# Kernel tuning notes

Hardware: AMD Instinct MI355X
Metric: run time of the kernel (lower is better)

Reference implementation:

```python
import jax, jax.numpy as jnp
import numpy as np

S = 2        # downscale
REDUCE = 32  # QK channel dim


def _to_grid(x):
    # [B,C,H,W] -> [B,C,H/S,W/S,S*S], matching ConverToGrid (reshape+permute+reshape)
    B, C, H, W = x.shape
    h, w = H // S, W // S
    x = x.reshape(B, C, h, S, w, S)
    x = x.transpose(0, 1, 2, 4, 3, 5)
    return x.reshape(B, C, h, w, S * S)


def setup_inputs() -> dict:
    key = jax.random.key(0)
    k1, k2, k3 = jax.random.split(key, 3)
    fm = jax.random.normal(k1, (8, 128, 256, 256), dtype=jnp.float32)
    Wq = jax.random.normal(k2, (REDUCE, 128), dtype=jnp.float32) * 0.05
    Wk = jax.random.normal(k3, (REDUCE, 128), dtype=jnp.float32) * 0.05
    return {"fm": fm, "Wq": Wq, "Wk": Wk}


def reference(fm, Wq, Wk):
    B, C, H, W = fm.shape
    h, w = H // S, W // S
    # Q branch: AvgPool2d(S,S) -> 1x1 conv -> scale by 1/sqrt(reduce)
    pooled = fm.reshape(B, C, h, S, w, S).mean(axis=(3, 5))          # [B,C,h,w]
    Q = jnp.einsum('rc,bchw->brhw', Wq, pooled) / jnp.sqrt(
        jnp.asarray(REDUCE, fm.dtype))                               # [B,r,h,w]
    # K branch: 1x1 conv -> grid
    K = _to_grid(jnp.einsum('rc,bchw->brhw', Wk, fm))                # [B,r,h,w,S*S]
    # V branch: grid of raw features
    V = _to_grid(fm)                                                 # [B,C,h,w,S*S]
    # sum over channel dim of Q*K, softmax over window dim (dropout p=0 => identity)
    logits = jnp.einsum('brhw,brhws->bhws', Q, K)                    # [B,h,w,S*S]
    attn = jax.nn.softmax(logits, axis=-1)
    # weighted sum over window positions
    out = jnp.einsum('bchws,bhws->bchw', V, attn)                    # [B,C,h,w]
    return out
```

## Files before the change

kernel.cpp:

```cpp
#include <hip/hip_runtime.h>
#include <hip/hip_bf16.h>
#include <math.h>


typedef unsigned int uint32;

__device__ __forceinline__ uint32 pack2(float x, float y) {
  union { __hip_bfloat162 h; uint32 u; } cvt;
  cvt.h = __float22bfloat162_rn(make_float2(x, y));
  return cvt.u;
}
__device__ __forceinline__ float2 unpack2(uint32 u) {
  float2 r;
  r.x = __uint_as_float(u << 16);
  r.y = __uint_as_float(u & 0xffff0000u);
  return r;
}

__global__ __launch_bounds__(256) void wt_kernel(const float* __restrict__ Wq,
                                                 const float* __restrict__ Wk,
                                                 float* __restrict__ ws) {
  int t = blockIdx.x * 256 + threadIdx.x;
  if (t < 4096) {
    int c = t >> 5, r = t & 31;
    ws[c * 32 + r]        = Wq[r * 128 + c] * (0.25f / sqrtf(32.0f));
    ws[4096 + c * 32 + r] = Wk[r * 128 + c];
  }
}

__global__ __launch_bounds__(256)
void attn_main(const float* __restrict__ fm,
               const float* __restrict__ ws,
               float* __restrict__ out) {
  __shared__ uint2 stash[128][64];
  __shared__ float lbuf[4][64][4];
  __shared__ float abuf[64][4];

  const int tid = threadIdx.x;
  const int p   = tid & 63;
  const int w   = __builtin_amdgcn_readfirstlane(tid >> 6);

  const int blk = blockIdx.x;
  const int w0  = (blk & 1) * 64;
  const int h   = (blk >> 1) & 127;
  const int b   = blk >> 8;

  const float* g = fm + ((size_t)(b * 128)) * 65536 +
                   (size_t)(2 * h) * 256 + 2 * (w0 + p);
  const float* wq = ws + 8 * w;
  const float* wk = ws + 4096 + 8 * w;

  float Kacc[8][4];
  float Qacc[8];
#pragma unroll
  for (int r = 0; r < 8; ++r) {
    Qacc[r] = 0.f;
    Kacc[r][0] = Kacc[r][1] = Kacc[r][2] = Kacc[r][3] = 0.f;
  }

  float2 ra[8], rb[8];
#pragma unroll
  for (int i = 0; i < 8; ++i) {
    ra[i] = *(const float2*)(g + (size_t)i * 65536);
    rb[i] = *(const float2*)(g + (size_t)i * 65536 + 256);
  }

  for (int c0 = 0; c0 < 128; c0 += 8) {
    const bool pf = (c0 < 120);
#pragma unroll
    for (int j = 0; j < 8; ++j) {
      const int c = c0 + j;
      const float2 va = ra[j];
      const float2 vb = rb[j];
      if (pf) {
        ra[j] = *(const float2*)(g + (size_t)(c + 8) * 65536);
        rb[j] = *(const float2*)(g + (size_t)(c + 8) * 65536 + 256);
      }
      stash[c][p] = make_uint2(pack2(va.x, va.y), pack2(vb.x, vb.y));
      const float u = (va.x + va.y) + (vb.x + vb.y);
#pragma unroll
      for (int r = 0; r < 8; ++r) {
        const float wqv = wq[c * 32 + r];
        const float wkv = wk[c * 32 + r];
        Qacc[r] = fmaf(wqv, u, Qacc[r]);
        Kacc[r][0] = fmaf(wkv, va.x, Kacc[r][0]);
        Kacc[r][1] = fmaf(wkv, va.y, Kacc[r][1]);
        Kacc[r][2] = fmaf(wkv, vb.x, Kacc[r][2]);
        Kacc[r][3] = fmaf(wkv, vb.y, Kacc[r][3]);
      }
    }
  }

  {
    float pl0 = 0.f, pl1 = 0.f, pl2 = 0.f, pl3 = 0.f;
#pragma unroll
    for (int r = 0; r < 8; ++r) {
      pl0 = fmaf(Qacc[r], Kacc[r][0], pl0);
      pl1 = fmaf(Qacc[r], Kacc[r][1], pl1);
      pl2 = fmaf(Qacc[r], Kacc[r][2], pl2);
      pl3 = fmaf(Qacc[r], Kacc[r][3], pl3);
    }
    *(float4*)&lbuf[w][p][0] = make_float4(pl0, pl1, pl2, pl3);
  }
  __syncthreads();

  if (tid < 64) {
    const float4 s0 = *(const float4*)&lbuf[0][tid][0];
    const float4 s1 = *(const float4*)&lbuf[1][tid][0];
    const float4 s2 = *(const float4*)&lbuf[2][tid][0];
    const float4 s3 = *(const float4*)&lbuf[3][tid][0];
    const float L0 = (s0.x + s1.x) + (s2.x + s3.x);
    const float L1 = (s0.y + s1.y) + (s2.y + s3.y);
    const float L2 = (s0.z + s1.z) + (s2.z + s3.z);
    const float L3 = (s0.w + s1.w) + (s2.w + s3.w);
    const float mx = fmaxf(fmaxf(L0, L1), fmaxf(L2, L3));
    const float e0 = __expf(L0 - mx), e1 = __expf(L1 - mx);
    const float e2 = __expf(L2 - mx), e3 = __expf(L3 - mx);
    const float inv = 1.0f / ((e0 + e1) + (e2 + e3));
    *(float4*)&abuf[tid][0] =
        make_float4(e0 * inv, e1 * inv, e2 * inv, e3 * inv);
  }
  __syncthreads();

  {
    const float4 at = *(const float4*)&abuf[p][0];
    const int cb = 32 * w;
    float* op = out + ((size_t)(b * 128 + cb)) * 16384 + h * 128 + w0 + p;
#pragma unroll 8
    for (int i = 0; i < 32; ++i) {
      const uint2 q = stash[cb + i][p];
      const float2 va = unpack2(q.x);
      const float2 vb = unpack2(q.y);
      op[(size_t)i * 16384] =
          fmaf(at.x, va.x, fmaf(at.y, va.y, fmaf(at.z, vb.x, at.w * vb.y)));
    }
  }
}

extern "C" void kernel_launch(void* const* d_in, const int* in_sizes, int n_in,
                              void* d_out, int out_size, void* d_ws, size_t ws_size,
                              hipStream_t stream) {
  const float* fm = (const float*)d_in[0];
  const float* Wq = (const float*)d_in[1];
  const float* Wk = (const float*)d_in[2];
  float* outp = (float*)d_out;
  float* ws = (float*)d_ws;

  wt_kernel<<<16, 256, 0, stream>>>(Wq, Wk, ws);
  attn_main<<<2048, 256, 0, stream>>>(fm, ws, outp);
}
```

Measured before the change: 146.8 us.

## Split channel ownership across waves and reassociate logits via Wk^T Q

Each wave now loads only its 32 channels of the feature map into the bf16 LDS stash, instead of every wave streaming all 128 channels. Q is then built cooperatively through LDS atomics. Logits are computed as sum over c of (Wk^T q)[c] * v[c], so the per-channel K projection is replaced by a projected query dotted with the stashed values. Weights are staged into LDS with global_load_lds in four chunks, which adds several barriers and raises dynamic LDS use to 80 KB per block. That LDS budget can limit occupancy, and the logits now come from bf16-rounded values.

```diff
diff --git a/kernel.cpp b/kernel.cpp
--- a/kernel.cpp
+++ b/kernel.cpp
@@ -4,6 +4,8 @@
 
 
 typedef unsigned int uint32;
+typedef const __attribute__((address_space(1))) void* gas_t;
+typedef __attribute__((address_space(3))) void* las_t;
 
 __device__ __forceinline__ uint32 pack2(float x, float y) {
   union { __hip_bfloat162 h; uint32 u; } cvt;
@@ -23,8 +25,9 @@
   int t = blockIdx.x * 256 + threadIdx.x;
   if (t < 4096) {
     int c = t >> 5, r = t & 31;
-    ws[c * 32 + r]        = Wq[r * 128 + c] * (0.25f / sqrtf(32.0f));
-    ws[4096 + c * 32 + r] = Wk[r * 128 + c];
+    int half = r >> 4, rr = r & 15;
+    ws[half * 2048 + c * 16 + rr] = Wq[r * 128 + c] * (0.25f / sqrtf(32.0f));
+    ws[4096 + half * 2048 + c * 16 + rr] = Wk[r * 128 + c];
   }
 }
 
@@ -32,83 +35,184 @@
 void attn_main(const float* __restrict__ fm,
                const float* __restrict__ ws,
                float* __restrict__ out) {
-  __shared__ uint2 stash[128][64];
-  __shared__ float lbuf[4][64][4];
-  __shared__ float abuf[64][4];
+  extern __shared__ char smem[];
+  uint2* stash = (uint2*)smem;
+  float* wbuf  = (float*)(smem + 65536);
+  float* Qbuf  = (float*)(smem + 73728);
+  float* lbuf  = Qbuf;
+  float* abuf  = Qbuf + 1024;
 
   const int tid = threadIdx.x;
   const int p   = tid & 63;
   const int w   = __builtin_amdgcn_readfirstlane(tid >> 6);
+  const int cb  = 32 * w;
 
   const int blk = blockIdx.x;
   const int w0  = (blk & 1) * 64;
   const int h   = (blk >> 1) & 127;
   const int b   = blk >> 8;
 
-  const float* g = fm + ((size_t)(b * 128)) * 65536 +
-                   (size_t)(2 * h) * 256 + 2 * (w0 + p);
-  const float* wq = ws + 8 * w;
-  const float* wk = ws + 4096 + 8 * w;
-
-  float Kacc[8][4];
-  float Qacc[8];
-#pragma unroll
-  for (int r = 0; r < 8; ++r) {
-    Qacc[r] = 0.f;
-    Kacc[r][0] = Kacc[r][1] = Kacc[r][2] = Kacc[r][3] = 0.f;
-  }
-
-  float2 ra[8], rb[8];
-#pragma unroll
-  for (int i = 0; i < 8; ++i) {
-    ra[i] = *(const float2*)(g + (size_t)i * 65536);
-    rb[i] = *(const float2*)(g + (size_t)i * 65536 + 256);
-  }
-
-  for (int c0 = 0; c0 < 128; c0 += 8) {
-    const bool pf = (c0 < 120);
-#pragma unroll
-    for (int j = 0; j < 8; ++j) {
-      const int c = c0 + j;
-      const float2 va = ra[j];
-      const float2 vb = rb[j];
-      if (pf) {
-        ra[j] = *(const float2*)(g + (size_t)(c + 8) * 65536);
-        rb[j] = *(const float2*)(g + (size_t)(c + 8) * 65536 + 256);
-      }
-      stash[c][p] = make_uint2(pack2(va.x, va.y), pack2(vb.x, vb.y));
-      const float u = (va.x + va.y) + (vb.x + vb.y);
-#pragma unroll
-      for (int r = 0; r < 8; ++r) {
-        const float wqv = wq[c * 32 + r];
-        const float wkv = wk[c * 32 + r];
-        Qacc[r] = fmaf(wqv, u, Qacc[r]);
-        Kacc[r][0] = fmaf(wkv, va.x, Kacc[r][0]);
-        Kacc[r][1] = fmaf(wkv, va.y, Kacc[r][1]);
-        Kacc[r][2] = fmaf(wkv, vb.x, Kacc[r][2]);
-        Kacc[r][3] = fmaf(wkv, vb.y, Kacc[r][3]);
+#pragma unroll
+  for (int j = 0; j < 8; ++j) Qbuf[tid * 8 + j] = 0.f;
+
+#define STAGE(koff)                                                          \
+  {                                                                          \
+    const char* src = (const char*)ws + (koff) + tid * 16;                   \
+    char* dst = (char*)wbuf + tid * 16;                                      \
+    __builtin_amdgcn_global_load_lds((gas_t)src, (las_t)dst, 16, 0, 0);      \
+    __builtin_amdgcn_global_load_lds((gas_t)(src + 4096), (las_t)(dst + 4096),\
+                                     16, 0, 0);                              \
+  }
+
+  STAGE(0)
+
+  {
+    const float* g = fm + ((size_t)(b * 128 + cb)) * 65536 +
+                     (size_t)(2 * h) * 256 + 2 * (w0 + p);
+    float2 ra[8], rb[8];
+#pragma unroll
+    for (int i = 0; i < 8; ++i) {
+      ra[i] = *(const float2*)(g + (size_t)i * 65536);
+      rb[i] = *(const float2*)(g + (size_t)i * 65536 + 256);
+    }
+#pragma unroll
+    for (int c0 = 0; c0 < 32; c0 += 8) {
+#pragma unroll
+      for (int j = 0; j < 8; ++j) {
+        const float2 va = ra[j];
+        const float2 vb = rb[j];
+        if (c0 < 24) {
+          ra[j] = *(const float2*)(g + (size_t)(c0 + 8 + j) * 65536);
+          rb[j] = *(const float2*)(g + (size_t)(c0 + 8 + j) * 65536 + 256);
+        }
+        stash[(cb + c0 + j) * 64 + p] =
+            make_uint2(pack2(va.x, va.y), pack2(vb.x, vb.y));
       }
     }
   }
-
-  {
-    float pl0 = 0.f, pl1 = 0.f, pl2 = 0.f, pl3 = 0.f;
-#pragma unroll
-    for (int r = 0; r < 8; ++r) {
-      pl0 = fmaf(Qacc[r], Kacc[r][0], pl0);
-      pl1 = fmaf(Qacc[r], Kacc[r][1], pl1);
-      pl2 = fmaf(Qacc[r], Kacc[r][2], pl2);
-      pl3 = fmaf(Qacc[r], Kacc[r][3], pl3);
-    }
-    *(float4*)&lbuf[w][p][0] = make_float4(pl0, pl1, pl2, pl3);
-  }
+  asm volatile("s_waitcnt vmcnt(0)" ::: "memory");
+  __syncthreads();
+
+  float Qacc[16];
+#pragma unroll
+  for (int r = 0; r < 16; ++r) Qacc[r] = 0.f;
+#pragma unroll
+  for (int c = 0; c < 32; ++c) {
+    const int cc = cb + c;
+    const uint2 sv = stash[cc * 64 + p];
+    const float2 va = unpack2(sv.x);
+    const float2 vb = unpack2(sv.y);
+    const float u = (va.x + va.y) + (vb.x + vb.y);
+    const float4 w0_ = *(const float4*)(wbuf + cc * 16 + 0);
+    const float4 w1_ = *(const float4*)(wbuf + cc * 16 + 4);
+    const float4 w2_ = *(const float4*)(wbuf + cc * 16 + 8);
+    const float4 w3_ = *(const float4*)(wbuf + cc * 16 + 12);
+    Qacc[0]  = fmaf(w0_.x, u, Qacc[0]);  Qacc[1]  = fmaf(w0_.y, u, Qacc[1]);
+    Qacc[2]  = fmaf(w0_.z, u, Qacc[2]);  Qacc[3]  = fmaf(w0_.w, u, Qacc[3]);
+    Qacc[4]  = fmaf(w1_.x, u, Qacc[4]);  Qacc[5]  = fmaf(w1_.y, u, Qacc[5]);
+    Qacc[6]  = fmaf(w1_.z, u, Qacc[6]);  Qacc[7]  = fmaf(w1_.w, u, Qacc[7]);
+    Qacc[8]  = fmaf(w2_.x, u, Qacc[8]);  Qacc[9]  = fmaf(w2_.y, u, Qacc[9]);
+    Qacc[10] = fmaf(w2_.z, u, Qacc[10]); Qacc[11] = fmaf(w2_.w, u, Qacc[11]);
+    Qacc[12] = fmaf(w3_.x, u, Qacc[12]); Qacc[13] = fmaf(w3_.y, u, Qacc[13]);
+    Qacc[14] = fmaf(w3_.z, u, Qacc[14]); Qacc[15] = fmaf(w3_.w, u, Qacc[15]);
+  }
+  __syncthreads();
+  STAGE(8192)
+#pragma unroll
+  for (int r = 0; r < 16; ++r) atomicAdd(&Qbuf[r * 64 + p], Qacc[r]);
+  asm volatile("s_waitcnt vmcnt(0)" ::: "memory");
+  __syncthreads();
+
+#pragma unroll
+  for (int r = 0; r < 16; ++r) Qacc[r] = 0.f;
+#pragma unroll
+  for (int c = 0; c < 32; ++c) {
+    const int cc = cb + c;
+    const uint2 sv = stash[cc * 64 + p];
+    const float2 va = unpack2(sv.x);
+    const float2 vb = unpack2(sv.y);
+    const float u = (va.x + va.y) + (vb.x + vb.y);
+    const float4 w0_ = *(const float4*)(wbuf + cc * 16 + 0);
+    const float4 w1_ = *(const float4*)(wbuf + cc * 16 + 4);
+    const float4 w2_ = *(const float4*)(wbuf + cc * 16 + 8);
+    const float4 w3_ = *(const float4*)(wbuf + cc * 16 + 12);
+    Qacc[0]  = fmaf(w0_.x, u, Qacc[0]);  Qacc[1]  = fmaf(w0_.y, u, Qacc[1]);
+    Qacc[2]  = fmaf(w0_.z, u, Qacc[2]);  Qacc[3]  = fmaf(w0_.w, u, Qacc[3]);
+    Qacc[4]  = fmaf(w1_.x, u, Qacc[4]);  Qacc[5]  = fmaf(w1_.y, u, Qacc[5]);
+    Qacc[6]  = fmaf(w1_.z, u, Qacc[6]);  Qacc[7]  = fmaf(w1_.w, u, Qacc[7]);
+    Qacc[8]  = fmaf(w2_.x, u, Qacc[8]);  Qacc[9]  = fmaf(w2_.y, u, Qacc[9]);
+    Qacc[10] = fmaf(w2_.z, u, Qacc[10]); Qacc[11] = fmaf(w2_.w, u, Qacc[11]);
+    Qacc[12] = fmaf(w3_.x, u, Qacc[12]); Qacc[13] = fmaf(w3_.y, u, Qacc[13]);
+    Qacc[14] = fmaf(w3_.z, u, Qacc[14]); Qacc[15] = fmaf(w3_.w, u, Qacc[15]);
+  }
+  __syncthreads();
+  STAGE(16384)
+#pragma unroll
+  for (int r = 0; r < 16; ++r) atomicAdd(&Qbuf[(16 + r) * 64 + p], Qacc[r]);
+  asm volatile("s_waitcnt vmcnt(0)" ::: "memory");
+  __syncthreads();
+
+  float qh[32];
+#pragma unroll
+  for (int r = 0; r < 32; ++r) qh[r] = Qbuf[r * 64 + p];
+
+  float tpart[32];
+#pragma unroll
+  for (int c = 0; c < 32; ++c) {
+    const int cc = cb + c;
+    const float4 k0 = *(const float4*)(wbuf + cc * 16 + 0);
+    const float4 k1 = *(const float4*)(wbuf + cc * 16 + 4);
+    const float4 k2 = *(const float4*)(wbuf + cc * 16 + 8);
+    const float4 k3 = *(const float4*)(wbuf + cc * 16 + 12);
+    float t0 = qh[0] * k0.x, t1 = qh[1] * k0.y;
+    t0 = fmaf(qh[2],  k0.z, t0); t1 = fmaf(qh[3],  k0.w, t1);
+    t0 = fmaf(qh[4],  k1.x, t0); t1 = fmaf(qh[5],  k1.y, t1);
+    t0 = fmaf(qh[6],  k1.z, t0); t1 = fmaf(qh[7],  k1.w, t1);
+    t0 = fmaf(qh[8],  k2.x, t0); t1 = fmaf(qh[9],  k2.y, t1);
+    t0 = fmaf(qh[10], k2.z, t0); t1 = fmaf(qh[11], k2.w, t1);
+    t0 = fmaf(qh[12], k3.x, t0); t1 = fmaf(qh[13], k3.y, t1);
+    t0 = fmaf(qh[14], k3.z, t0); t1 = fmaf(qh[15], k3.w, t1);
+    tpart[c] = t0 + t1;
+  }
+  __syncthreads();
+  STAGE(24576)
+  asm volatile("s_waitcnt vmcnt(0)" ::: "memory");
+  __syncthreads();
+
+  float l0 = 0.f, l1 = 0.f, l2 = 0.f, l3 = 0.f;
+#pragma unroll
+  for (int c = 0; c < 32; ++c) {
+    const int cc = cb + c;
+    const float4 k0 = *(const float4*)(wbuf + cc * 16 + 0);
+    const float4 k1 = *(const float4*)(wbuf + cc * 16 + 4);
+    const float4 k2 = *(const float4*)(wbuf + cc * 16 + 8);
+    const float4 k3 = *(const float4*)(wbuf + cc * 16 + 12);
+    float t0 = qh[16] * k0.x, t1 = qh[17] * k0.y;
+    t0 = fmaf(qh[18], k0.z, t0); t1 = fmaf(qh[19], k0.w, t1);
+    t0 = fmaf(qh[20], k1.x, t0); t1 = fmaf(qh[21], k1.y, t1);
+    t0 = fmaf(qh[22], k1.z, t0); t1 = fmaf(qh[23], k1.w, t1);
+    t0 = fmaf(qh[24], k2.x, t0); t1 = fmaf(qh[25], k2.y, t1);
+    t0 = fmaf(qh[26], k2.z, t0); t1 = fmaf(qh[27], k2.w, t1);
+    t0 = fmaf(qh[28], k3.x, t0); t1 = fmaf(qh[29], k3.y, t1);
+    t0 = fmaf(qh[30], k3.z, t0); t1 = fmaf(qh[31], k3.w, t1);
+    const float tv = tpart[c] + (t0 + t1);
+    const uint2 sv = stash[cc * 64 + p];
+    const float2 va = unpack2(sv.x);
+    const float2 vb = unpack2(sv.y);
+    l0 = fmaf(tv, va.x, l0);
+    l1 = fmaf(tv, va.y, l1);
+    l2 = fmaf(tv, vb.x, l2);
+    l3 = fmaf(tv, vb.y, l3);
+  }
+  __syncthreads();
+  *(float4*)(lbuf + (w * 64 + p) * 4) = make_float4(l0, l1, l2, l3);
   __syncthreads();
 
   if (tid < 64) {
-    const float4 s0 = *(const float4*)&lbuf[0][tid][0];
-    const float4 s1 = *(const float4*)&lbuf[1][tid][0];
-    const float4 s2 = *(const float4*)&lbuf[2][tid][0];
-    const float4 s3 = *(const float4*)&lbuf[3][tid][0];
+    const float4 s0 = *(const float4*)(lbuf + (0 * 64 + tid) * 4);
+    const float4 s1 = *(const float4*)(lbuf + (1 * 64 + tid) * 4);
+    const float4 s2 = *(const float4*)(lbuf + (2 * 64 + tid) * 4);
+    const float4 s3 = *(const float4*)(lbuf + (3 * 64 + tid) * 4);
     const float L0 = (s0.x + s1.x) + (s2.x + s3.x);
     const float L1 = (s0.y + s1.y) + (s2.y + s3.y);
     const float L2 = (s0.z + s1.z) + (s2.z + s3.z);
@@ -117,24 +221,24 @@
     const float e0 = __expf(L0 - mx), e1 = __expf(L1 - mx);
     const float e2 = __expf(L2 - mx), e3 = __expf(L3 - mx);
     const float inv = 1.0f / ((e0 + e1) + (e2 + e3));
-    *(float4*)&abuf[tid][0] =
+    *(float4*)(abuf + tid * 4) =
         make_float4(e0 * inv, e1 * inv, e2 * inv, e3 * inv);
   }
   __syncthreads();
 
   {
-    const float4 at = *(const float4*)&abuf[p][0];
-    const int cb = 32 * w;
+    const float4 at = *(const float4*)(abuf + p * 4);
     float* op = out + ((size_t)(b * 128 + cb)) * 16384 + h * 128 + w0 + p;
 #pragma unroll 8
-    for (int i = 0; i < 32; ++i) {
-      const uint2 q = stash[cb + i][p];
-      const float2 va = unpack2(q.x);
-      const float2 vb = unpack2(q.y);
-      op[(size_t)i * 16384] =
+    for (int c = 0; c < 32; ++c) {
+      const uint2 sv = stash[(cb + c) * 64 + p];
+      const float2 va = unpack2(sv.x);
+      const float2 vb = unpack2(sv.y);
+      op[(size_t)c * 16384] =
           fmaf(at.x, va.x, fmaf(at.y, va.y, fmaf(at.z, vb.x, at.w * vb.y)));
     }
   }
+#undef STAGE
 }
 
 extern "C" void kernel_launch(void* const* d_in, const int* in_sizes, int n_in,
@@ -146,6 +250,11 @@
   float* outp = (float*)d_out;
   float* ws = (float*)d_ws;
 
+  const int smem_bytes = 81920;
+  (void)hipFuncSetAttribute((const void*)attn_main,
+                            hipFuncAttributeMaxDynamicSharedMemorySize,
+                            smem_bytes);
+
   wt_kernel<<<16, 256, 0, stream>>>(Wq, Wk, ws);
-  attn_main<<<2048, 256, 0, stream>>>(fm, ws, outp);
-}
+  attn_main<<<2048, 256, smem_bytes, stream>>>(fm, ws, outp);
+}
```

Result: slower. 374.6 us (+155.2%).
